# Kernel optimization log

Hardware: AMD Instinct MI355X
Metric: run time of the kernel (lower is better)

Reference implementation:

```python
import jax, jax.numpy as jnp
import numpy as np

N = 100000
E = 1600000
DIN = 128
H = 64
L = 2  # num_layer


def setup_inputs() -> dict:
    key = jax.random.key(0)
    ks = jax.random.split(key, 10)
    x = jax.random.normal(ks[0], (N, DIN), dtype=jnp.float32)
    edge_index = jax.random.randint(ks[1], (2, E), 0, N, dtype=jnp.int64)
    edge_attr = jax.random.uniform(ks[2], (E,), dtype=jnp.float32)
    batch = jnp.zeros((N,), dtype=jnp.int64)
    s_in = 1.0 / np.sqrt(DIN)
    s_h = 1.0 / np.sqrt(H)
    W_emb = jax.random.normal(ks[3], (DIN, H), dtype=jnp.float32) * s_in
    b_emb = jnp.zeros((H,), dtype=jnp.float32)
    # Stacked per-layer LEConv params: lin1 (W1,b1), lin2 (W2, no bias), lin3 (W3,b3)
    W1 = jax.random.normal(ks[4], (L, H, H), dtype=jnp.float32) * s_h
    b1 = jnp.zeros((L, H), dtype=jnp.float32)
    W2 = jax.random.normal(ks[5], (L, H, H), dtype=jnp.float32) * s_h
    W3 = jax.random.normal(ks[6], (L, H, H), dtype=jnp.float32) * s_h
    b3 = jnp.zeros((L, H), dtype=jnp.float32)
    return {"x": x, "edge_index": edge_index, "edge_attr": edge_attr, "batch": batch,
            "W_emb": W_emb, "b_emb": b_emb, "W1": W1, "b1": b1, "W2": W2,
            "W3": W3, "b3": b3}


def reference(x, edge_index, edge_attr, batch, W_emb, b_emb, W1, b1, W2, W3, b3):
    # node embedding
    h = x @ W_emb + b_emb  # [N, H]
    src = edge_index[0]  # message source j
    dst = edge_index[1]  # aggregation target i
    w = edge_attr[:, None]  # [E, 1]
    for l in range(L):
        a = h @ W1[l] + b1[l]          # lin1(x)
        b = h @ W2[l]                  # lin2(x), no bias
        # LEConv message: e_ji * (a_j - b_i), aggregated at i
        msg = (a[src] - b[dst]) * w    # [E, H]
        agg = jax.ops.segment_sum(msg, dst, num_segments=N)
        h = agg + h @ W3[l] + b3[l]    # + lin3(x)
        # dropout (eval mode => identity), then ReLU
        h = jax.nn.relu(h)
    return h
```

## Files before the change

kernel.cpp:

```cpp
#include <hip/hip_runtime.h>

#define NNODES 100000
#define NEDGES 1600000
#define DINP   128
#define HDIM   64
#define NLAYERS 2

#define NBUCK 256
#define BDIV  391
#define TILE  8192
#define NT    ((NEDGES + TILE - 1) / TILE)
#define NTOT  (NBUCK * NT)
#define SEG   (NTOT / 1024)
#define EMB_BLOCKS 1563

typedef unsigned short ushort_t;
typedef unsigned int   uint_t;
typedef unsigned char  uchar_t;
typedef __attribute__((ext_vector_type(8))) short bf16x8;
typedef __attribute__((ext_vector_type(4))) float f32x4;
typedef __attribute__((ext_vector_type(2))) float f32x2;

__device__ __forceinline__ ushort_t f32_to_bf16_rne(float x) {
    uint_t u = __float_as_uint(x);
    u = (u + 0x7FFFu + ((u >> 16) & 1u)) >> 16;
    return (ushort_t)u;
}
__device__ __forceinline__ float bf16_to_f32(ushort_t v) {
    return __uint_as_float(((uint_t)v) << 16);
}
__device__ __forceinline__ uint_t pack_bf16(float lo, float hi) {
    return (uint_t)f32_to_bf16_rne(lo) | ((uint_t)f32_to_bf16_rne(hi) << 16);
}


__global__ __launch_bounds__(256) void wprep_all(
    const float* __restrict__ Wemb, const float* __restrict__ W1,
    const float* __restrict__ W2, const float* __restrict__ W3,
    ushort_t* __restrict__ wefrag, ushort_t* __restrict__ wfrag)
{
    int t = blockIdx.x * 256 + threadIdx.x;
    if (t < 8192) {
        int j  = t & 7;
        int l  = (t >> 3) & 63;
        int nt = (t >> 9) & 3;
        int kb = (t >> 11) & 3;
        int k = kb * 32 + 8 * (l >> 4) + j;
        int n = nt * 16 + (l & 15);
        float w = Wemb[k * HDIM + n];
        ushort_t hi = f32_to_bf16_rne(w);
        ushort_t lo = f32_to_bf16_rne(w - bf16_to_f32(hi));
        wefrag[(((0 * 4 + kb) * 4 + nt) * 64 + l) * 8 + j] = hi;
        wefrag[(((1 * 4 + kb) * 4 + nt) * 64 + l) * 8 + j] = lo;
    } else {
        int u = t - 8192;
        if (u >= 2 * 3 * 2 * 4 * 64 * 8) return;
        int j    = u & 7;
        int l    = (u >> 3) & 63;
        int nt   = (u >> 9) & 3;
        int kb   = (u >> 11) & 1;
        int mat  = (u >> 12) % 3;
        int layer = u / 12288;
        int kp = kb * 32 + 8 * (l >> 4) + j;
        int k  = (kp & 3) * 16 + (kp >> 2);
        int n = nt * 16 + (l & 15);
        const float* Wm = (mat == 0) ? W1 : (mat == 1) ? W2 : W3;
        float w = Wm[(size_t)layer * HDIM * HDIM + k * HDIM + n];
        ushort_t hi = f32_to_bf16_rne(w);
        ushort_t lo = f32_to_bf16_rne(w - bf16_to_f32(hi));
        size_t base = (size_t)layer * 24576;
        wfrag[base + ((((size_t)(mat * 2 + 0) * 2 + kb) * 4 + nt) * 64 + l) * 8 + j] = hi;
        wfrag[base + ((((size_t)(mat * 2 + 1) * 2 + kb) * 4 + nt) * 64 + l) * 8 + j] = lo;
    }
}

__global__ __launch_bounds__(256) void emb_p1(
    const float* __restrict__ x, const ushort_t* __restrict__ wefrag,
    const float* __restrict__ bemb, ushort_t* __restrict__ hbf,
    uchar_t* __restrict__ hq8,
    const int* __restrict__ dst, int* __restrict__ tileOff)
{
    __shared__ int hist[NBUCK];
    if (blockIdx.x < EMB_BLOCKS) {
        const int wid = blockIdx.x * 4 + (threadIdx.x >> 6);
        if (wid >= NNODES / 16) return;
        const int lane = threadIdx.x & 63;
        const int lrow = lane & 15;
        const int lgrp = lane >> 4;
        const int r0 = wid * 16;

        f32x4 acc[4];
#pragma unroll
        for (int nt = 0; nt < 4; ++nt) acc[nt] = (f32x4){0.f, 0.f, 0.f, 0.f};

#pragma unroll
        for (int kb = 0; kb < 4; ++kb) {
            const float* xp = x + (size_t)(r0 + lrow) * DINP + kb * 32 + lgrp * 8;
            float4 xa = *(const float4*)xp;
            float4 xb = *(const float4*)(xp + 4);
            bf16x8 xhi;
            xhi[0] = (short)f32_to_bf16_rne(xa.x);
            xhi[1] = (short)f32_to_bf16_rne(xa.y);
            xhi[2] = (short)f32_to_bf16_rne(xa.z);
            xhi[3] = (short)f32_to_bf16_rne(xa.w);
            xhi[4] = (short)f32_to_bf16_rne(xb.x);
            xhi[5] = (short)f32_to_bf16_rne(xb.y);
            xhi[6] = (short)f32_to_bf16_rne(xb.z);
            xhi[7] = (short)f32_to_bf16_rne(xb.w);
#pragma unroll
            for (int nt = 0; nt < 4; ++nt) {
                bf16x8 bhi = *(const bf16x8*)(wefrag + (((0 * 4 + kb) * 4 + nt) * 64 + lane) * 8);
                bf16x8 blo = *(const bf16x8*)(wefrag + (((1 * 4 + kb) * 4 + nt) * 64 + lane) * 8);
                acc[nt] = __builtin_amdgcn_mfma_f32_16x16x32_bf16(xhi, bhi, acc[nt], 0, 0, 0);
                acc[nt] = __builtin_amdgcn_mfma_f32_16x16x32_bf16(xhi, blo, acc[nt], 0, 0, 0);
            }
        }

        float bv[4];
#pragma unroll
        for (int nt = 0; nt < 4; ++nt) bv[nt] = bemb[nt * 16 + lrow];

#pragma unroll
        for (int r = 0; r < 4; ++r) {
            int row = r0 + lgrp * 4 + r;
            float o[4];
#pragma unroll
            for (int nt = 0; nt < 4; ++nt) o[nt] = acc[nt][r] + bv[nt];
            uint2 hb;
            hb.x = pack_bf16(o[0], o[1]);
            hb.y = pack_bf16(o[2], o[3]);
            *(uint2*)(hbf + ((size_t)row << 6) + (lrow << 2)) = hb;
            int q = __builtin_amdgcn_cvt_pk_fp8_f32(o[0], o[1], 0, false);
            q = __builtin_amdgcn_cvt_pk_fp8_f32(o[2], o[3], q, true);
            *(int*)(hq8 + ((size_t)row << 6) + (lrow << 2)) = q;
        }
    } else {
        const int tl = blockIdx.x - EMB_BLOCKS, t = threadIdx.x;
        hist[t] = 0;
        __syncthreads();
        const int base = tl * TILE;
#pragma unroll
        for (int i = 0; i < TILE / 256; ++i) {
            int e = base + i * 256 + t;
            if (e < NEDGES) atomicAdd(&hist[dst[e] / BDIV], 1);
        }
        __syncthreads();
        tileOff[t * NT + tl] = hist[t];
    }
}

__global__ __launch_bounds__(1024) void p2_scan(int* __restrict__ tileOff)
{
    __shared__ int sd[1024];
    const int t = threadIdx.x;
    const int lo = t * SEG;
    int s = 0;
    for (int i = 0; i < SEG; ++i) s += tileOff[lo + i];
    sd[t] = s;
    __syncthreads();
    for (int off = 1; off < 1024; off <<= 1) {
        int v = (t >= off) ? sd[t - off] : 0;
        __syncthreads();
        sd[t] += v;
        __syncthreads();
    }
    int run = sd[t] - s;
    for (int i = 0; i < SEG; ++i) {
        int c = tileOff[lo + i];
        tileOff[lo + i] = run;
        run += c;
    }
}

__global__ __launch_bounds__(256) void p3_bin(
    const int* __restrict__ src, const int* __restrict__ dst,
    const float* __restrict__ attr, const int* __restrict__ tileOff,
    int2* __restrict__ tmp)
{
    __shared__ int cur[NBUCK];
    const int tl = blockIdx.x, t = threadIdx.x;
    cur[t] = tileOff[t * NT + tl];
    __syncthreads();
#pragma unroll
    for (int i = 0; i < TILE / 256; ++i) {
        int e = tl * TILE + i * 256 + t;
        if (e < NEDGES) {
            int d  = dst[e];
            int bk = d / BDIV;
            int ld = d - bk * BDIV;
            int pos = atomicAdd(&cur[bk], 1);
            int2 p;
            p.x = (ld << 17) | src[e];
            p.y = __float_as_int(attr[e]);
            tmp[pos] = p;
        }
    }
}

__global__ __launch_bounds__(256) void p4_sort(
    const int2* __restrict__ tmp, const int* __restrict__ tileOff,
    int2* __restrict__ edgeS, int* __restrict__ rowptr,
    float* __restrict__ degw)
{
    __shared__ int sdh[512];
    __shared__ int cur[BDIV + 1];
    __shared__ float sdw[BDIV];
    const int b = blockIdx.x, t = threadIdx.x;
    const int n0 = b * BDIV;
    const int nn = (NNODES - n0 < BDIV) ? (NNODES - n0) : BDIV;
    const int ebeg = tileOff[b * NT];
    const int eend = (b + 1 < NBUCK) ? tileOff[(b + 1) * NT] : NEDGES;

    sdh[t] = 0; sdh[t + 256] = 0;
    for (int i = t; i < BDIV; i += 256) sdw[i] = 0.f;
    __syncthreads();
    for (int e = ebeg + t; e < eend; e += 256)
        atomicAdd(&sdh[tmp[e].x >> 17], 1);
    __syncthreads();
    for (int off = 1; off < 512; off <<= 1) {
        int i0 = t, i1 = t + 256;
        int v0 = (i0 >= off) ? sdh[i0 - off] : 0;
        int v1 = (i1 >= off) ? sdh[i1 - off] : 0;
        __syncthreads();
        sdh[i0] += v0; sdh[i1] += v1;
        __syncthreads();
    }
    for (int i = t; i < nn; i += 256) {
        int c = ebeg + (i ? sdh[i - 1] : 0);
        cur[i] = c;
        rowptr[n0 + i] = c;
    }
    if (b == NBUCK - 1 && t == 0) rowptr[NNODES] = NEDGES;
    __syncthreads();
    for (int e = ebeg + t; e < eend; e += 256) {
        int2 w = tmp[e];
        int ld = w.x >> 17;
        int pos = atomicAdd(&cur[ld], 1);
        atomicAdd(&sdw[ld], __int_as_float(w.y));
        int2 p;
        p.x = (w.x & 0x1FFFF) << 6;
        p.y = w.y;
        edgeS[pos] = p;
    }
    __syncthreads();
    for (int i = t; i < nn; i += 256) degw[n0 + i] = sdw[i];
}

__global__ __launch_bounds__(256) void gather_kernel(
    const int* __restrict__ rowptr, const int2* __restrict__ edgeS,
    const uchar_t* __restrict__ hq8, ushort_t* __restrict__ aggbf)
{
    const int v   = blockIdx.x * 8 + (threadIdx.x >> 5);
    const int t5  = threadIdx.x & 31;
    const int oct = t5 >> 3;
    const int ol  = t5 & 7;
    const int beg = rowptr[v], end = rowptr[v + 1];
    const int cnt = end - beg;
    const uchar_t* __restrict__ hq8o = hq8 + (ol << 3);
    const int2* __restrict__ ep = edgeS + beg + oct;

    float a0 = 0.f, a1 = 0.f, a2 = 0.f, a3 = 0.f;
    float a4 = 0.f, a5 = 0.f, a6 = 0.f, a7 = 0.f;
    const int nfull = cnt >> 2;
#pragma unroll 2
    for (int k = 0; k < nfull; ++k) {
        int2 ev = ep[(size_t)k * 4];
        float wv = __int_as_float(ev.y);
        uint2 u = *(const uint2*)(hq8o + ev.x);
        f32x2 f01 = __builtin_amdgcn_cvt_pk_f32_fp8((int)u.x, false);
        f32x2 f23 = __builtin_amdgcn_cvt_pk_f32_fp8((int)u.x, true);
        f32x2 f45 = __builtin_amdgcn_cvt_pk_f32_fp8((int)u.y, false);
        f32x2 f67 = __builtin_amdgcn_cvt_pk_f32_fp8((int)u.y, true);
        a0 += wv * f01[0];  a1 += wv * f01[1];
        a2 += wv * f23[0];  a3 += wv * f23[1];
        a4 += wv * f45[0];  a5 += wv * f45[1];
        a6 += wv * f67[0];  a7 += wv * f67[1];
    }
    if (cnt & 3) {
        int idx = beg + (nfull << 2) + oct;
        bool ok = idx < end;
        int2 ev = edgeS[ok ? idx : beg];
        float wv = ok ? __int_as_float(ev.y) : 0.f;
        uint2 u = *(const uint2*)(hq8o + ev.x);
        f32x2 f01 = __builtin_amdgcn_cvt_pk_f32_fp8((int)u.x, false);
        f32x2 f23 = __builtin_amdgcn_cvt_pk_f32_fp8((int)u.x, true);
        f32x2 f45 = __builtin_amdgcn_cvt_pk_f32_fp8((int)u.y, false);
        f32x2 f67 = __builtin_amdgcn_cvt_pk_f32_fp8((int)u.y, true);
        a0 += wv * f01[0];  a1 += wv * f01[1];
        a2 += wv * f23[0];  a3 += wv * f23[1];
        a4 += wv * f45[0];  a5 += wv * f45[1];
        a6 += wv * f67[0];  a7 += wv * f67[1];
    }

    a0 += __shfl_xor(a0, 8); a0 += __shfl_xor(a0, 16);
    a1 += __shfl_xor(a1, 8); a1 += __shfl_xor(a1, 16);
    a2 += __shfl_xor(a2, 8); a2 += __shfl_xor(a2, 16);
    a3 += __shfl_xor(a3, 8); a3 += __shfl_xor(a3, 16);
    a4 += __shfl_xor(a4, 8); a4 += __shfl_xor(a4, 16);
    a5 += __shfl_xor(a5, 8); a5 += __shfl_xor(a5, 16);
    a6 += __shfl_xor(a6, 8); a6 += __shfl_xor(a6, 16);
    a7 += __shfl_xor(a7, 8); a7 += __shfl_xor(a7, 16);

    if (oct == 0) {
        uint4 o;
        o.x = pack_bf16(a0, a1);
        o.y = pack_bf16(a2, a3);
        o.z = pack_bf16(a4, a5);
        o.w = pack_bf16(a6, a7);
        *(uint4*)(aggbf + ((size_t)v << 6) + (ol << 3)) = o;
    }
}

template<int WRITE_BF>
__global__ __launch_bounds__(256) void dense_mfma(
    const ushort_t* __restrict__ hbf, const ushort_t* __restrict__ aggbf,
    const float* __restrict__ degw, const ushort_t* __restrict__ wfrag,
    const float* __restrict__ b1, const float* __restrict__ b3,
    float* __restrict__ hout, ushort_t* __restrict__ hbf_out,
    uchar_t* __restrict__ hq8_out)
{
    const int wid = blockIdx.x * 4 + (threadIdx.x >> 6);
    if (wid >= NNODES / 16) return;
    const int lane = threadIdx.x & 63;
    const int lrow = lane & 15;
    const int lgrp = lane >> 4;
    const int r0   = wid * 16;

    f32x4 acc[3][4];
#pragma unroll
    for (int m = 0; m < 3; ++m)
#pragma unroll
        for (int nt = 0; nt < 4; ++nt)
            acc[m][nt] = (f32x4){0.f, 0.f, 0.f, 0.f};

#pragma unroll
    for (int kb = 0; kb < 2; ++kb) {
        const size_t aoff = ((size_t)(r0 + lrow) << 6) + kb * 32 + lgrp * 8;
        bf16x8 a_agg = *(const bf16x8*)(aggbf + aoff);
        bf16x8 a_h   = *(const bf16x8*)(hbf + aoff);
#pragma unroll
        for (int mv = 0; mv < 6; ++mv) {
            const int mat = mv >> 1;
            bf16x8 a = (mat == 0) ? a_agg : a_h;
            const ushort_t* wb = wfrag + (((size_t)mv * 2 + kb) * 4) * 512 + lane * 8;
#pragma unroll
            for (int nt = 0; nt < 4; ++nt) {
                bf16x8 b = *(const bf16x8*)(wb + nt * 512);
                acc[mat][nt] = __builtin_amdgcn_mfma_f32_16x16x32_bf16(
                    a, b, acc[mat][nt], 0, 0, 0);
            }
        }
    }

    float dreg[4];
#pragma unroll
    for (int r = 0; r < 4; ++r) dreg[r] = degw[r0 + lgrp * 4 + r];

    float b1v[4], b3v[4];
#pragma unroll
    for (int nt = 0; nt < 4; ++nt) {
        b1v[nt] = b1[nt * 16 + lrow];
        b3v[nt] = b3[nt * 16 + lrow];
    }

#pragma unroll
    for (int r = 0; r < 4; ++r) {
        int row = r0 + lgrp * 4 + r;
        float o[4];
#pragma unroll
        for (int nt = 0; nt < 4; ++nt) {
            float t = acc[0][nt][r] + acc[2][nt][r] - dreg[r] * acc[1][nt][r]
                    + dreg[r] * b1v[nt] + b3v[nt];
            o[nt] = fmaxf(t, 0.f);
        }
        if (WRITE_BF) {
            uint2 hb;
            hb.x = pack_bf16(o[0], o[1]);
            hb.y = pack_bf16(o[2], o[3]);
            *(uint2*)(hbf_out + ((size_t)row << 6) + (lrow << 2)) = hb;
            int q = __builtin_amdgcn_cvt_pk_fp8_f32(o[0], o[1], 0, false);
            q = __builtin_amdgcn_cvt_pk_fp8_f32(o[2], o[3], q, true);
            *(int*)(hq8_out + ((size_t)row << 6) + (lrow << 2)) = q;
        } else {
#pragma unroll
            for (int nt = 0; nt < 4; ++nt)
                hout[((size_t)row << 6) + nt * 16 + lrow] = o[nt];
        }
    }
}

extern "C" void kernel_launch(void* const* d_in, const int* in_sizes, int n_in,
                              void* d_out, int out_size, void* d_ws, size_t ws_size,
                              hipStream_t stream)
{
    const float* x    = (const float*)d_in[0];
    const int*   eidx = (const int*)  d_in[1];
    const float* attr = (const float*)d_in[2];
    const float* Wemb = (const float*)d_in[4];
    const float* bemb = (const float*)d_in[5];
    const float* W1   = (const float*)d_in[6];
    const float* b1   = (const float*)d_in[7];
    const float* W2   = (const float*)d_in[8];
    const float* W3   = (const float*)d_in[9];
    const float* b3   = (const float*)d_in[10];

    float* hout = (float*)d_out;

    float*    degw    = (float*)d_ws;
    int*      rowptr  = (int*)d_ws + 100000;
    int*      tileOff = (int*)d_ws + 200016;
    int2*     edgeS   = (int2*)((int*)d_ws + 250192);
    ushort_t* hbf     = (ushort_t*)((int*)d_ws + 3450192);
    ushort_t* aggbf   = (ushort_t*)((int*)d_ws + 6650192);
    int2*     tmp     = (int2*)aggbf;
    ushort_t* wfrag   = (ushort_t*)((int*)d_ws + 9850192);
    ushort_t* wefrag  = (ushort_t*)((int*)d_ws + 9874768);
    uchar_t*  hq8     = (uchar_t*)((int*)d_ws + 9882960);

    const int* srcI = eidx;
    const int* dstI = eidx + NEDGES;

    wprep_all<<<128, 256, 0, stream>>>(Wemb, W1, W2, W3, wefrag, wfrag);

    emb_p1<<<EMB_BLOCKS + NT, 256, 0, stream>>>(
        x, wefrag, bemb, hbf, hq8, dstI, tileOff);

    p2_scan<<<1, 1024, 0, stream>>>(tileOff);
    p3_bin <<<NT, 256, 0, stream>>>(srcI, dstI, attr, tileOff, tmp);
    p4_sort<<<NBUCK, 256, 0, stream>>>(tmp, tileOff, edgeS, rowptr, degw);

    const int mfmaGrid = (NNODES / 16 + 3) / 4;
    const int gatherGrid = NNODES / 8;
    gather_kernel<<<gatherGrid, 256, 0, stream>>>(rowptr, edgeS, hq8, aggbf);
    dense_mfma<1><<<mfmaGrid, 256, 0, stream>>>(
        hbf, aggbf, degw, wfrag, b1, b3, hout, hbf, hq8);
    gather_kernel<<<gatherGrid, 256, 0, stream>>>(rowptr, edgeS, hq8, aggbf);
    dense_mfma<0><<<mfmaGrid, 256, 0, stream>>>(
        hbf, aggbf, degw, wfrag + 24576, b1 + HDIM, b3 + HDIM, hout, hbf, hq8);
}
```

Before: 197.1 us.

## Split binning tiles across more blocks and narrow gather to 16 lanes per node

The binning pass now launches four blocks per edge tile and claims output slots with global atomics on per-bucket-per-tile cursors that the scan kernel seeds, instead of using shared-memory cursors. This gives the binning step more parallelism at the cost of contended global atomics. The gather kernel now assigns 16 lanes per node (two edge streams) instead of 32 (four streams), packing twice as many nodes per block and needing one fewer shuffle stage. That raises per-lane serial work per node but cuts idle lanes for low-degree nodes.

```diff
diff --git a/kernel.cpp b/kernel.cpp
--- a/kernel.cpp
+++ b/kernel.cpp
@@ -13,6 +13,8 @@
 #define NTOT  (NBUCK * NT)
 #define SEG   (NTOT / 1024)
 #define EMB_BLOCKS 1563
+#define SUBT 4
+#define SEGT (TILE / SUBT)
 
 typedef unsigned short ushort_t;
 typedef unsigned int   uint_t;
@@ -149,7 +151,8 @@
     }
 }
 
-__global__ __launch_bounds__(1024) void p2_scan(int* __restrict__ tileOff)
+__global__ __launch_bounds__(1024) void p2_scan(
+    int* __restrict__ tileOff, int* __restrict__ gcur)
 {
     __shared__ int sd[1024];
     const int t = threadIdx.x;
@@ -168,27 +171,28 @@
     for (int i = 0; i < SEG; ++i) {
         int c = tileOff[lo + i];
         tileOff[lo + i] = run;
+        gcur[lo + i] = run;
         run += c;
     }
 }
 
 __global__ __launch_bounds__(256) void p3_bin(
     const int* __restrict__ src, const int* __restrict__ dst,
-    const float* __restrict__ attr, const int* __restrict__ tileOff,
+    const float* __restrict__ attr, int* __restrict__ gcur,
     int2* __restrict__ tmp)
 {
-    __shared__ int cur[NBUCK];
-    const int tl = blockIdx.x, t = threadIdx.x;
-    cur[t] = tileOff[t * NT + tl];
-    __syncthreads();
-#pragma unroll
-    for (int i = 0; i < TILE / 256; ++i) {
-        int e = tl * TILE + i * 256 + t;
+    const int tl = blockIdx.x >> 2;
+    const int sb = blockIdx.x & 3;
+    const int base = tl * TILE + sb * SEGT;
+    const int t = threadIdx.x;
+#pragma unroll
+    for (int i = 0; i < SEGT / 256; ++i) {
+        int e = base + i * 256 + t;
         if (e < NEDGES) {
             int d  = dst[e];
             int bk = d / BDIV;
             int ld = d - bk * BDIV;
-            int pos = atomicAdd(&cur[bk], 1);
+            int pos = atomicAdd(&gcur[bk * NT + tl], 1);
             int2 p;
             p.x = (ld << 17) | src[e];
             p.y = __float_as_int(attr[e]);
@@ -250,10 +254,10 @@
     const int* __restrict__ rowptr, const int2* __restrict__ edgeS,
     const uchar_t* __restrict__ hq8, ushort_t* __restrict__ aggbf)
 {
-    const int v   = blockIdx.x * 8 + (threadIdx.x >> 5);
-    const int t5  = threadIdx.x & 31;
-    const int oct = t5 >> 3;
-    const int ol  = t5 & 7;
+    const int v   = blockIdx.x * 16 + (threadIdx.x >> 4);
+    const int t4  = threadIdx.x & 15;
+    const int oct = t4 >> 3;
+    const int ol  = t4 & 7;
     const int beg = rowptr[v], end = rowptr[v + 1];
     const int cnt = end - beg;
     const uchar_t* __restrict__ hq8o = hq8 + (ol << 3);
@@ -261,10 +265,10 @@
 
     float a0 = 0.f, a1 = 0.f, a2 = 0.f, a3 = 0.f;
     float a4 = 0.f, a5 = 0.f, a6 = 0.f, a7 = 0.f;
-    const int nfull = cnt >> 2;
+    const int nfull = cnt >> 1;
 #pragma unroll 2
     for (int k = 0; k < nfull; ++k) {
-        int2 ev = ep[(size_t)k * 4];
+        int2 ev = ep[(size_t)k * 2];
         float wv = __int_as_float(ev.y);
         uint2 u = *(const uint2*)(hq8o + ev.x);
         f32x2 f01 = __builtin_amdgcn_cvt_pk_f32_fp8((int)u.x, false);
@@ -276,8 +280,8 @@
         a4 += wv * f45[0];  a5 += wv * f45[1];
         a6 += wv * f67[0];  a7 += wv * f67[1];
     }
-    if (cnt & 3) {
-        int idx = beg + (nfull << 2) + oct;
+    if (cnt & 1) {
+        int idx = beg + (nfull << 1) + oct;
         bool ok = idx < end;
         int2 ev = edgeS[ok ? idx : beg];
         float wv = ok ? __int_as_float(ev.y) : 0.f;
@@ -292,14 +296,14 @@
         a6 += wv * f67[0];  a7 += wv * f67[1];
     }
 
-    a0 += __shfl_xor(a0, 8); a0 += __shfl_xor(a0, 16);
-    a1 += __shfl_xor(a1, 8); a1 += __shfl_xor(a1, 16);
-    a2 += __shfl_xor(a2, 8); a2 += __shfl_xor(a2, 16);
-    a3 += __shfl_xor(a3, 8); a3 += __shfl_xor(a3, 16);
-    a4 += __shfl_xor(a4, 8); a4 += __shfl_xor(a4, 16);
-    a5 += __shfl_xor(a5, 8); a5 += __shfl_xor(a5, 16);
-    a6 += __shfl_xor(a6, 8); a6 += __shfl_xor(a6, 16);
-    a7 += __shfl_xor(a7, 8); a7 += __shfl_xor(a7, 16);
+    a0 += __shfl_xor(a0, 8);
+    a1 += __shfl_xor(a1, 8);
+    a2 += __shfl_xor(a2, 8);
+    a3 += __shfl_xor(a3, 8);
+    a4 += __shfl_xor(a4, 8);
+    a5 += __shfl_xor(a5, 8);
+    a6 += __shfl_xor(a6, 8);
+    a7 += __shfl_xor(a7, 8);
 
     if (oct == 0) {
         uint4 o;
@@ -416,6 +420,7 @@
     ushort_t* wfrag   = (ushort_t*)((int*)d_ws + 9850192);
     ushort_t* wefrag  = (ushort_t*)((int*)d_ws + 9874768);
     uchar_t*  hq8     = (uchar_t*)((int*)d_ws + 9882960);
+    int*      gcur    = (int*)d_ws + 11482960;
 
     const int* srcI = eidx;
     const int* dstI = eidx + NEDGES;
@@ -425,12 +430,12 @@
     emb_p1<<<EMB_BLOCKS + NT, 256, 0, stream>>>(
         x, wefrag, bemb, hbf, hq8, dstI, tileOff);
 
-    p2_scan<<<1, 1024, 0, stream>>>(tileOff);
-    p3_bin <<<NT, 256, 0, stream>>>(srcI, dstI, attr, tileOff, tmp);
+    p2_scan<<<1, 1024, 0, stream>>>(tileOff, gcur);
+    p3_bin <<<NT * SUBT, 256, 0, stream>>>(srcI, dstI, attr, gcur, tmp);
     p4_sort<<<NBUCK, 256, 0, stream>>>(tmp, tileOff, edgeS, rowptr, degw);
 
     const int mfmaGrid = (NNODES / 16 + 3) / 4;
-    const int gatherGrid = NNODES / 8;
+    const int gatherGrid = NNODES / 16;
     gather_kernel<<<gatherGrid, 256, 0, stream>>>(rowptr, edgeS, hq8, aggbf);
     dense_mfma<1><<<mfmaGrid, 256, 0, stream>>>(
         hbf, aggbf, degw, wfrag, b1, b3, hout, hbf, hq8);
```

After: 303.2 us. 53.8% more time.
